# Performance work log

Measured on AMD Instinct MI355X. Metric: run time of the kernel, lower is better.

Reference implementation:

```python
import jax, jax.numpy as jnp
import numpy as np

B, N, D, DH, H, L = 32768, 6, 128, 64, 4, 4  # batch, items, dim_inp, head/ffn dim, heads, encoders
SEQ = 4  # tokens kept by embeddings[:, :4, :]
EPS = 1e-5


def _layernorm(x, g, b):
    mu = jnp.mean(x, axis=-1, keepdims=True)
    var = jnp.mean((x - mu) ** 2, axis=-1, keepdims=True)
    return (x - mu) / jnp.sqrt(var + EPS) * g + b


def setup_inputs() -> dict:
    key = jax.random.key(0)
    ks = jax.random.split(key, 18)
    s = 0.05
    f32 = jnp.float32
    return {
        "embeddings": jax.random.normal(ks[0], (B, N, D), f32),
        # per-layer, per-head QKV projections: [L, H, D, DH]
        "wq": jax.random.normal(ks[1], (L, H, D, DH), f32) * s,
        "bq": jax.random.normal(ks[2], (L, H, DH), f32) * s,
        "wk": jax.random.normal(ks[3], (L, H, D, DH), f32) * s,
        "bk": jax.random.normal(ks[4], (L, H, DH), f32) * s,
        "wv": jax.random.normal(ks[5], (L, H, D, DH), f32) * s,
        "bv": jax.random.normal(ks[6], (L, H, DH), f32) * s,
        # output projection after head concat: [L, H*DH, D]
        "wo": jax.random.normal(ks[7], (L, H * DH, D), f32) * s,
        "bo": jax.random.normal(ks[8], (L, D), f32) * s,
        "ln1_g": jnp.ones((L, D), f32),
        "ln1_b": jnp.zeros((L, D), f32),
        # FFN: Linear(D, DH) -> GELU -> Linear(DH, D)
        "ff_w1": jax.random.normal(ks[9], (L, D, DH), f32) * s,
        "ff_b1": jax.random.normal(ks[10], (L, DH), f32) * s,
        "ff_w2": jax.random.normal(ks[11], (L, DH, D), f32) * s,
        "ff_b2": jax.random.normal(ks[12], (L, D), f32) * s,
        "ln2_g": jnp.ones((L, D), f32),
        "ln2_b": jnp.zeros((L, D), f32),
    }


def reference(embeddings, wq, bq, wk, bk, wv, bv, wo, bo,
              ln1_g, ln1_b, ff_w1, ff_b1, ff_w2, ff_b2, ln2_g, ln2_b):
    x = embeddings[:, :SEQ, :]          # [B, 4, D]
    positive_pair = embeddings[:, 4, :]  # [B, D]
    negative_pairs = embeddings[:, 5:, :]  # [B, 1, D]

    # Original AttentionHead scales by sqrt(seq_len) (query.size(1)), not sqrt(head_dim)
    scale = jnp.sqrt(jnp.asarray(SEQ, x.dtype))

    for l in range(L):
        # all heads batched into one einsum (same math as per-head Linear+bmm loop)
        q = jnp.einsum('bsd,hdf->bhsf', x, wq[l]) + bq[l][:, None, :]
        k = jnp.einsum('bsd,hdf->bhsf', x, wk[l]) + bk[l][:, None, :]
        v = jnp.einsum('bsd,hdf->bhsf', x, wv[l]) + bv[l][:, None, :]
        scores = jnp.einsum('bhsf,bhtf->bhst', q, k) / scale  # [B,H,4,4]
        attn = jax.nn.softmax(scores, axis=-1)
        ctx = jnp.einsum('bhst,bhtf->bhsf', attn, v)
        # torch.cat over heads along last dim == [B,S,H,DH] -> [B,S,H*DH]
        ctx = ctx.transpose(0, 2, 1, 3).reshape(x.shape[0], SEQ, H * DH)
        proj = ctx @ wo[l] + bo[l]
        context = _layernorm(x + proj, ln1_g[l], ln1_b[l])
        # FFN (dropout = identity in eval); GELU is exact (erf) as in torch default
        h = jax.nn.gelu(context @ ff_w1[l] + ff_b1[l], approximate=False)
        res = h @ ff_w2[l] + ff_b2[l]
        # NOTE: residual uses the PRE-attention input (faithful to Encoder.forward)
        x = _layernorm(res + x, ln2_g[l], ln2_b[l])

    final_embedding = x.mean(axis=-2)  # [B, D]
    return (final_embedding, positive_pair, negative_pairs)
```

## Files before the change

kernel.cpp:

```cpp
#include <hip/hip_runtime.h>
#include <stdint.h>


typedef __attribute__((ext_vector_type(8))) short    bf16x8;
typedef __attribute__((ext_vector_type(4))) _Float16 f16x4;
typedef __attribute__((ext_vector_type(4))) float    f32x4;

#define MFMA_BF(a,b,c) __builtin_amdgcn_mfma_f32_16x16x32_bf16((a),(b),(c),0,0,0)
#define MFMA_H(a,b,c)  __builtin_amdgcn_mfma_f32_16x16x16f16((a),(b),(c),0,0,0)

__device__ __forceinline__ unsigned short f2bf(float f){
  unsigned u = __float_as_uint(f);
  u += 0x7FFFu + ((u>>16)&1u);
  return (unsigned short)(u>>16);
}
__device__ __forceinline__ unsigned pk2bf(float a, float b){
  return (unsigned)f2bf(a) | ((unsigned)f2bf(b)<<16);
}
__device__ __forceinline__ unsigned pkh(float a, float b){
  auto h = __builtin_amdgcn_cvt_pkrtz(a, b);
  return __builtin_bit_cast(unsigned, h);
}
__device__ __forceinline__ void ubf2(unsigned u, float& a, float& b){
  a = __uint_as_float(u<<16);
  b = __uint_as_float(u & 0xffff0000u);
}

__global__ __launch_bounds__(256) void prep_kernel(
    const float* __restrict__ wq, const float* __restrict__ wk,
    const float* __restrict__ wv, const float* __restrict__ wo,
    const float* __restrict__ w1, const float* __restrict__ w2,
    unsigned short* __restrict__ ws){
  int e16 = blockIdx.x*256 + threadIdx.x;
  int t    = e16 >> 10;
  int c    = (e16 >> 6) & 15;
  int lane = e16 & 63;
  int lnid = lane & 15, qid = lane >> 4;
  int l = t/18, r = t - l*18;
  float v[8];
  if (r < 16){
    int h = r >> 2, ty = r & 3;
    if (ty < 3){
      const float* W = (ty==0? wq : (ty==1? wk : wv)) + (size_t)(l*4+h)*8192;
      int f = (c>>2)*16 + lnid, d0 = (c&3)*32 + qid*8;
      #pragma unroll
      for (int j=0;j<8;++j) v[j] = W[(d0+j)*64 + f];
    } else {
      const float* W = wo + (size_t)l*32768 + (size_t)h*8192;
      int dd = (c>>1)*16 + lnid, k0 = (c&1)*32 + qid*8;
      #pragma unroll
      for (int j=0;j<8;++j) v[j] = W[(k0+j)*128 + dd];
    }
  } else if (r == 16){
    const float* W = w1 + (size_t)l*8192;
    int f = (c>>2)*16 + lnid, d0 = (c&3)*32 + qid*8;
    #pragma unroll
    for (int j=0;j<8;++j) v[j] = W[(d0+j)*64 + f];
  } else {
    const float* W = w2 + (size_t)l*8192;
    int dd = (c>>1)*16 + lnid, k0 = (c&1)*32 + qid*8;
    #pragma unroll
    for (int j=0;j<8;++j) v[j] = W[(k0+j)*128 + dd];
  }
  uint4 o;
  o.x = pk2bf(v[0],v[1]); o.y = pk2bf(v[2],v[3]);
  o.z = pk2bf(v[4],v[5]); o.w = pk2bf(v[6],v[7]);
  ((uint4*)ws)[e16] = o;
}

#define XOFF  0
#define QOFF  4352
#define KOFF  6656
#define VOFF  8960
#define PG    11520
#define WSOFF 46080
#define SLOTSZ 16384
#define LDSSZ 78848

__global__ __launch_bounds__(256,2) void bert_kernel(
    const float* __restrict__ emb,
    const float* __restrict__ bq, const float* __restrict__ bk, const float* __restrict__ bv,
    const float* __restrict__ bo,
    const float* __restrict__ ln1g, const float* __restrict__ ln1b,
    const float* __restrict__ fb1, const float* __restrict__ fb2,
    const float* __restrict__ ln2g, const float* __restrict__ ln2b,
    const unsigned short* __restrict__ ws,
    float* __restrict__ out)
{
  __shared__ __align__(16) char smem[LDSSZ];
  const int tid  = threadIdx.x;
  const int wid  = tid>>6;
  const int lane = tid&63;
  const int lnid = lane&15;
  const int qid  = lane>>4;
  const int batch0 = blockIdx.x*16;
  char* gb = smem + wid*PG;
  const f32x4 ZV = {0.f,0.f,0.f,0.f};

  {
    int row = lane>>2, colq = (lane&3)*32;
    const float* src = emb + ((size_t)(batch0 + wid*4 + (row>>2))*6 + (row&3))*128 + colq;
    #pragma unroll
    for (int i=0;i<8;++i){
      float4 v = *(const float4*)(src + i*4);
      uint2 u; u.x = pk2bf(v.x,v.y); u.y = pk2bf(v.z,v.w);
      *(uint2*)(gb + XOFF + row*272 + (colq+i*4)*2) = u;
    }
  }
  {
    const float* eb = emb + (size_t)batch0*768;
    float* o1 = out + 4194304 + (size_t)batch0*128;
    float* o2 = out + 8388608 + (size_t)batch0*128;
    #pragma unroll
    for (int i=0;i<4;++i){
      int idx = i*256 + tid;
      int b = idx>>6, rem = idx&63;
      float4 v = *(const float4*)(eb + b*768 + 512 + rem*4);
      if (rem<32) *(float4*)(o1 + b*128 + rem*4) = v;
      else        *(float4*)(o2 + b*128 + (rem-32)*4) = v;
    }
  }

  const uint4* wsv = (const uint4*)ws;
  {
    #pragma unroll
    for (int i=0;i<4;++i)
      *(uint4*)(smem + WSOFF + (i*256+tid)*16) = wsv[i*256+tid];
  }
  __syncthreads();

  f32x4  pacc[8];
  bf16x8 xfrag[4];
  f16x4  vreg[4];
  int sidx = 0;

  for (int l=0; l<4; ++l){
    #pragma unroll
    for (int kc=0;kc<4;++kc)
      xfrag[kc] = *(const bf16x8*)(gb + XOFF + lnid*272 + kc*64 + qid*16);
    #pragma unroll
    for (int nt=0;nt<8;++nt) pacc[nt] = ZV;

    for (int ph=0; ph<18; ++ph){
      char* slot = smem + WSOFF + (sidx&1)*SLOTSZ;

      uint4 pf0,pf1,pf2,pf3;
      bool havepf = (sidx+1 < 72);
      if (havepf){
        const uint4* p = wsv + (size_t)(sidx+1)*1024 + tid;
        pf0 = p[0]; pf1 = p[256]; pf2 = p[512]; pf3 = p[768];
      }

      if (ph < 16){
        int h = ph>>2, t = ph&3;
        if (t < 2){
          char* dst = gb + (t? KOFF : QOFF);
          const float* bias_base = (t? bk : bq) + (l*4+h)*64;
          #pragma unroll
          for (int nt=0; nt<4; ++nt){
            f32x4 a = ZV;
            #pragma unroll
            for (int kc=0; kc<4; ++kc){
              bf16x8 wf = *(const bf16x8*)(slot + (nt*4+kc)*1024 + lane*16);
              a = MFMA_BF(wf, xfrag[kc], a);
            }
            f32x4 bs = *(const f32x4*)(bias_base + nt*16 + qid*4);
            uint2 u; u.x = pk2bf(a[0]+bs[0], a[1]+bs[1]);
                     u.y = pk2bf(a[2]+bs[2], a[3]+bs[3]);
            *(uint2*)(dst + lnid*144 + nt*32 + qid*8) = u;
          }
        } else if (t == 2){
          const float* bias_base = bv + (l*4+h)*64;
          #pragma unroll
          for (int nt=0; nt<4; ++nt){
            f32x4 a = ZV;
            #pragma unroll
            for (int kc=0; kc<4; ++kc){
              bf16x8 wf = *(const bf16x8*)(slot + (nt*4+kc)*1024 + lane*16);
              a = MFMA_BF(xfrag[kc], wf, a);
            }
            float b = bias_base[nt*16 + lnid];
            union { unsigned u[2]; f16x4 h4; } pu;
            pu.u[0] = pkh(a[0]+b, a[1]+b);
            pu.u[1] = pkh(a[2]+b, a[3]+b);
            vreg[nt] = pu.h4;
          }
        } else {
          bf16x8 kf0 = *(const bf16x8*)(gb+KOFF + lnid*144 + qid*16);
          bf16x8 kf1 = *(const bf16x8*)(gb+KOFF + lnid*144 + 64 + qid*16);
          bf16x8 qf0 = *(const bf16x8*)(gb+QOFF + lnid*144 + qid*16);
          bf16x8 qf1 = *(const bf16x8*)(gb+QOFF + lnid*144 + 64 + qid*16);
          f32x4 st = MFMA_BF(kf0, qf0, ZV);
          st = MFMA_BF(kf1, qf1, st);
          float s0=st[0]*0.5f, s1=st[1]*0.5f, s2=st[2]*0.5f, s3=st[3]*0.5f;
          float mx = fmaxf(fmaxf(s0,s1), fmaxf(s2,s3));
          float p0=__expf(s0-mx), p1=__expf(s1-mx), p2=__expf(s2-mx), p3=__expf(s3-mx);
          float inv = 1.f/(p0+p1+p2+p3);
          bool valid = (lnid>>2) == qid;
          p0 = valid? p0*inv:0.f; p1 = valid? p1*inv:0.f;
          p2 = valid? p2*inv:0.f; p3 = valid? p3*inv:0.f;
          union { unsigned u[2]; f16x4 h4; } pu;
          pu.u[0] = pkh(p0,p1);
          pu.u[1] = pkh(p2,p3);
          f16x4 pf = pu.h4;
          #pragma unroll
          for (int ft=0; ft<4; ++ft){
            f32x4 c = MFMA_H(vreg[ft], pf, ZV);
            uint2 u; u.x = pk2bf(c[0],c[1]); u.y = pk2bf(c[2],c[3]);
            *(uint2*)(gb+QOFF + lnid*144 + ft*32 + qid*8) = u;
          }
          asm volatile("" ::: "memory");
          bf16x8 c0 = *(const bf16x8*)(gb+QOFF + lnid*144 + qid*16);
          bf16x8 c1 = *(const bf16x8*)(gb+QOFF + lnid*144 + 64 + qid*16);
          #pragma unroll
          for (int nt=0; nt<8; ++nt){
            bf16x8 w0 = *(const bf16x8*)(slot + (nt*2+0)*1024 + lane*16);
            bf16x8 w1f= *(const bf16x8*)(slot + (nt*2+1)*1024 + lane*16);
            f32x4 a = pacc[nt];
            a = MFMA_BF(w0, c0, a);
            a = MFMA_BF(w1f, c1, a);
            pacc[nt] = a;
          }
        }
      } else if (ph == 16){
        float sm=0.f, sq=0.f;
        #pragma unroll
        for (int nt=0;nt<8;++nt){
          f32x4 b4 = *(const f32x4*)(bo + l*128 + nt*16 + qid*4);
          uint2 xr = *(const uint2*)(gb+XOFF + lnid*272 + nt*32 + qid*8);
          float x0,x1,x2,x3; ubf2(xr.x,x0,x1); ubf2(xr.y,x2,x3);
          f32x4 a = pacc[nt];
          a[0]+=b4[0]+x0; a[1]+=b4[1]+x1; a[2]+=b4[2]+x2; a[3]+=b4[3]+x3;
          sm += a[0]+a[1]+a[2]+a[3];
          sq += a[0]*a[0]+a[1]*a[1]+a[2]*a[2]+a[3]*a[3];
          pacc[nt] = a;
        }
        sm += __shfl_xor(sm,16); sq += __shfl_xor(sq,16);
        sm += __shfl_xor(sm,32); sq += __shfl_xor(sq,32);
        float mu = sm*(1.f/128.f);
        float rs = rsqrtf(sq*(1.f/128.f) - mu*mu + 1e-5f);
        #pragma unroll
        for (int nt=0;nt<8;++nt){
          f32x4 g4 = *(const f32x4*)(ln1g + l*128 + nt*16 + qid*4);
          f32x4 be = *(const f32x4*)(ln1b + l*128 + nt*16 + qid*4);
          f32x4 a = pacc[nt];
          float v0 = (a[0]-mu)*rs*g4[0]+be[0];
          float v1 = (a[1]-mu)*rs*g4[1]+be[1];
          float v2 = (a[2]-mu)*rs*g4[2]+be[2];
          float v3 = (a[3]-mu)*rs*g4[3]+be[3];
          uint2 u; u.x = pk2bf(v0,v1); u.y = pk2bf(v2,v3);
          *(uint2*)(gb+QOFF + lnid*272 + nt*32 + qid*8) = u;
        }
        asm volatile("" ::: "memory");
        bf16x8 x2f[4];
        #pragma unroll
        for (int kc=0;kc<4;++kc)
          x2f[kc] = *(const bf16x8*)(gb+QOFF + lnid*272 + kc*64 + qid*16);
        #pragma unroll
        for (int nt=0; nt<4; ++nt){
          f32x4 a = ZV;
          #pragma unroll
          for (int kc=0; kc<4; ++kc){
            bf16x8 wf = *(const bf16x8*)(slot + (nt*4+kc)*1024 + lane*16);
            a = MFMA_BF(wf, x2f[kc], a);
          }
          f32x4 b1 = *(const f32x4*)(fb1 + l*64 + nt*16 + qid*4);
          float g0,g1,g2,g3;
          { float x = a[0]+b1[0]; g0 = 0.5f*x*(1.f+erff(x*0.70710678f)); }
          { float x = a[1]+b1[1]; g1 = 0.5f*x*(1.f+erff(x*0.70710678f)); }
          { float x = a[2]+b1[2]; g2 = 0.5f*x*(1.f+erff(x*0.70710678f)); }
          { float x = a[3]+b1[3]; g3 = 0.5f*x*(1.f+erff(x*0.70710678f)); }
          uint2 u; u.x = pk2bf(g0,g1); u.y = pk2bf(g2,g3);
          *(uint2*)(gb+VOFF + lnid*144 + nt*32 + qid*8) = u;
        }
      } else {
        bf16x8 h0  = *(const bf16x8*)(gb+VOFF + lnid*144 + qid*16);
        bf16x8 h1f = *(const bf16x8*)(gb+VOFF + lnid*144 + 64 + qid*16);
        f32x4 racc[8];
        #pragma unroll
        for (int nt=0; nt<8; ++nt){
          bf16x8 w0 = *(const bf16x8*)(slot + (nt*2+0)*1024 + lane*16);
          bf16x8 w1f= *(const bf16x8*)(slot + (nt*2+1)*1024 + lane*16);
          f32x4 a = MFMA_BF(w0, h0, ZV);
          a = MFMA_BF(w1f, h1f, a);
          racc[nt] = a;
        }
        float sm=0.f, sq=0.f;
        #pragma unroll
        for (int nt=0;nt<8;++nt){
          f32x4 b4 = *(const f32x4*)(fb2 + l*128 + nt*16 + qid*4);
          uint2 xr = *(const uint2*)(gb+XOFF + lnid*272 + nt*32 + qid*8);
          float x0,x1,x2,x3; ubf2(xr.x,x0,x1); ubf2(xr.y,x2,x3);
          f32x4 a = racc[nt];
          a[0]+=b4[0]+x0; a[1]+=b4[1]+x1; a[2]+=b4[2]+x2; a[3]+=b4[3]+x3;
          sm += a[0]+a[1]+a[2]+a[3];
          sq += a[0]*a[0]+a[1]*a[1]+a[2]*a[2]+a[3]*a[3];
          racc[nt] = a;
        }
        sm += __shfl_xor(sm,16); sq += __shfl_xor(sq,16);
        sm += __shfl_xor(sm,32); sq += __shfl_xor(sq,32);
        float mu = sm*(1.f/128.f);
        float rs = rsqrtf(sq*(1.f/128.f) - mu*mu + 1e-5f);
        #pragma unroll
        for (int nt=0;nt<8;++nt){
          f32x4 g4 = *(const f32x4*)(ln2g + l*128 + nt*16 + qid*4);
          f32x4 be = *(const f32x4*)(ln2b + l*128 + nt*16 + qid*4);
          f32x4 a = racc[nt];
          float v0 = (a[0]-mu)*rs*g4[0]+be[0];
          float v1 = (a[1]-mu)*rs*g4[1]+be[1];
          float v2 = (a[2]-mu)*rs*g4[2]+be[2];
          float v3 = (a[3]-mu)*rs*g4[3]+be[3];
          uint2 u; u.x = pk2bf(v0,v1); u.y = pk2bf(v2,v3);
          *(uint2*)(gb+XOFF + lnid*272 + nt*32 + qid*8) = u;
        }
      }

      if (havepf){
        char* ns = smem + WSOFF + ((sidx+1)&1)*SLOTSZ;
        uint4* q = (uint4*)(ns) + tid;
        q[0]=pf0; q[256]=pf1; q[512]=pf2; q[768]=pf3;
      }
      __syncthreads();
      ++sidx;
    }
  }

  {
    int bl = lane>>4;
    float acc[8] = {0,0,0,0,0,0,0,0};
    #pragma unroll
    for (int s=0;s<4;++s){
      uint4 u = *(const uint4*)(gb + XOFF + (bl*4+s)*272 + lnid*16);
      float a0,a1;
      ubf2(u.x,a0,a1); acc[0]+=a0; acc[1]+=a1;
      ubf2(u.y,a0,a1); acc[2]+=a0; acc[3]+=a1;
      ubf2(u.z,a0,a1); acc[4]+=a0; acc[5]+=a1;
      ubf2(u.w,a0,a1); acc[6]+=a0; acc[7]+=a1;
    }
    float* dst = out + (size_t)(batch0 + wid*4 + bl)*128 + lnid*8;
    f32x4 v0 = {acc[0]*0.25f, acc[1]*0.25f, acc[2]*0.25f, acc[3]*0.25f};
    f32x4 v1 = {acc[4]*0.25f, acc[5]*0.25f, acc[6]*0.25f, acc[7]*0.25f};
    *(f32x4*)dst = v0;
    *(f32x4*)(dst+4) = v1;
  }
}

extern "C" void kernel_launch(void* const* d_in, const int* in_sizes, int n_in,
                              void* d_out, int out_size, void* d_ws, size_t ws_size,
                              hipStream_t stream) {
  const float* emb  = (const float*)d_in[0];
  const float* wq   = (const float*)d_in[1];
  const float* bq   = (const float*)d_in[2];
  const float* wk   = (const float*)d_in[3];
  const float* bk   = (const float*)d_in[4];
  const float* wv   = (const float*)d_in[5];
  const float* bv   = (const float*)d_in[6];
  const float* wo   = (const float*)d_in[7];
  const float* bo   = (const float*)d_in[8];
  const float* ln1g = (const float*)d_in[9];
  const float* ln1b = (const float*)d_in[10];
  const float* fw1  = (const float*)d_in[11];
  const float* fb1  = (const float*)d_in[12];
  const float* fw2  = (const float*)d_in[13];
  const float* fb2  = (const float*)d_in[14];
  const float* ln2g = (const float*)d_in[15];
  const float* ln2b = (const float*)d_in[16];
  unsigned short* ws = (unsigned short*)d_ws;
  float* out = (float*)d_out;

  prep_kernel<<<288, 256, 0, stream>>>(wq, wk, wv, wo, fw1, fw2, ws);
  bert_kernel<<<2048, 256, 0, stream>>>(emb, bq, bk, bv, bo, ln1g, ln1b,
                                        fb1, fb2, ln2g, ln2b, ws, out);
}
```

Baseline: 628.3 us.

## Single-buffer weight slot and reuse Q region to fit three blocks per CU

```diff
diff --git a/kernel.cpp b/kernel.cpp
--- a/kernel.cpp
+++ b/kernel.cpp
@@ -71,13 +71,12 @@
 #define XOFF  0
 #define QOFF  4352
 #define KOFF  6656
-#define VOFF  8960
-#define PG    11520
-#define WSOFF 46080
+#define PG    8960
+#define WSOFF 35840
 #define SLOTSZ 16384
-#define LDSSZ 78848
-
-__global__ __launch_bounds__(256,2) void bert_kernel(
+#define LDSSZ 52224
+
+__global__ __launch_bounds__(256,3) void bert_kernel(
     const float* __restrict__ emb,
     const float* __restrict__ bq, const float* __restrict__ bk, const float* __restrict__ bv,
     const float* __restrict__ bo,
@@ -95,7 +94,9 @@
   const int qid  = lane>>4;
   const int batch0 = blockIdx.x*16;
   char* gb = smem + wid*PG;
+  char* slot = smem + WSOFF;
   const f32x4 ZV = {0.f,0.f,0.f,0.f};
+  const uint4* wsv = (const uint4*)ws;
 
   {
     int row = lane>>2, colq = (lane&3)*32;
@@ -120,19 +121,16 @@
       else        *(float4*)(o2 + b*128 + (rem-32)*4) = v;
     }
   }
-
-  const uint4* wsv = (const uint4*)ws;
   {
     #pragma unroll
     for (int i=0;i<4;++i)
-      *(uint4*)(smem + WSOFF + (i*256+tid)*16) = wsv[i*256+tid];
+      *(uint4*)(slot + (i*256+tid)*16) = wsv[i*256+tid];
   }
   __syncthreads();
 
   f32x4  pacc[8];
   bf16x8 xfrag[4];
   f16x4  vreg[4];
-  int sidx = 0;
 
   for (int l=0; l<4; ++l){
     #pragma unroll
@@ -142,20 +140,25 @@
     for (int nt=0;nt<8;++nt) pacc[nt] = ZV;
 
     for (int ph=0; ph<18; ++ph){
-      char* slot = smem + WSOFF + (sidx&1)*SLOTSZ;
-
-      uint4 pf0,pf1,pf2,pf3;
-      bool havepf = (sidx+1 < 72);
+      const int nxt = l*18 + ph + 1;
+      const bool havepf = (nxt < 72);
+      uint4 pf0, pf1, pf2, pf3;
       if (havepf){
-        const uint4* p = wsv + (size_t)(sidx+1)*1024 + tid;
+        const uint4* p = wsv + (size_t)nxt*1024 + tid;
         pf0 = p[0]; pf1 = p[256]; pf2 = p[512]; pf3 = p[768];
       }
+      auto commit = [&](){
+        if (havepf){
+          uint4* q = (uint4*)slot + tid;
+          q[0]=pf0; q[256]=pf1; q[512]=pf2; q[768]=pf3;
+        }
+      };
 
       if (ph < 16){
         int h = ph>>2, t = ph&3;
         if (t < 2){
-          char* dst = gb + (t? KOFF : QOFF);
           const float* bias_base = (t? bk : bq) + (l*4+h)*64;
+          f32x4 a4[4];
           #pragma unroll
           for (int nt=0; nt<4; ++nt){
             f32x4 a = ZV;
@@ -164,13 +167,22 @@
               bf16x8 wf = *(const bf16x8*)(slot + (nt*4+kc)*1024 + lane*16);
               a = MFMA_BF(wf, xfrag[kc], a);
             }
+            a4[nt] = a;
+          }
+          __syncthreads();
+          commit();
+          char* dst = gb + (t? KOFF : QOFF);
+          #pragma unroll
+          for (int nt=0; nt<4; ++nt){
             f32x4 bs = *(const f32x4*)(bias_base + nt*16 + qid*4);
-            uint2 u; u.x = pk2bf(a[0]+bs[0], a[1]+bs[1]);
-                     u.y = pk2bf(a[2]+bs[2], a[3]+bs[3]);
+            uint2 u; u.x = pk2bf(a4[nt][0]+bs[0], a4[nt][1]+bs[1]);
+                     u.y = pk2bf(a4[nt][2]+bs[2], a4[nt][3]+bs[3]);
             *(uint2*)(dst + lnid*144 + nt*32 + qid*8) = u;
           }
+          __syncthreads();
         } else if (t == 2){
           const float* bias_base = bv + (l*4+h)*64;
+          f32x4 a4[4];
           #pragma unroll
           for (int nt=0; nt<4; ++nt){
             f32x4 a = ZV;
@@ -179,12 +191,19 @@
               bf16x8 wf = *(const bf16x8*)(slot + (nt*4+kc)*1024 + lane*16);
               a = MFMA_BF(xfrag[kc], wf, a);
             }
+            a4[nt] = a;
+          }
+          __syncthreads();
+          commit();
+          #pragma unroll
+          for (int nt=0; nt<4; ++nt){
             float b = bias_base[nt*16 + lnid];
             union { unsigned u[2]; f16x4 h4; } pu;
-            pu.u[0] = pkh(a[0]+b, a[1]+b);
-            pu.u[1] = pkh(a[2]+b, a[3]+b);
+            pu.u[0] = pkh(a4[nt][0]+b, a4[nt][1]+b);
+            pu.u[1] = pkh(a4[nt][2]+b, a4[nt][3]+b);
             vreg[nt] = pu.h4;
           }
+          __syncthreads();
         } else {
           bf16x8 kf0 = *(const bf16x8*)(gb+KOFF + lnid*144 + qid*16);
           bf16x8 kf1 = *(const bf16x8*)(gb+KOFF + lnid*144 + 64 + qid*16);
@@ -221,6 +240,9 @@
             a = MFMA_BF(w1f, c1, a);
             pacc[nt] = a;
           }
+          __syncthreads();
+          commit();
+          __syncthreads();
         }
       } else if (ph == 16){
         float sm=0.f, sq=0.f;
@@ -256,6 +278,7 @@
         #pragma unroll
         for (int kc=0;kc<4;++kc)
           x2f[kc] = *(const bf16x8*)(gb+QOFF + lnid*272 + kc*64 + qid*16);
+        f32x4 f14[4];
         #pragma unroll
         for (int nt=0; nt<4; ++nt){
           f32x4 a = ZV;
@@ -264,18 +287,26 @@
             bf16x8 wf = *(const bf16x8*)(slot + (nt*4+kc)*1024 + lane*16);
             a = MFMA_BF(wf, x2f[kc], a);
           }
+          f14[nt] = a;
+        }
+        __syncthreads();
+        commit();
+        #pragma unroll
+        for (int nt=0; nt<4; ++nt){
           f32x4 b1 = *(const f32x4*)(fb1 + l*64 + nt*16 + qid*4);
+          f32x4 a = f14[nt];
           float g0,g1,g2,g3;
           { float x = a[0]+b1[0]; g0 = 0.5f*x*(1.f+erff(x*0.70710678f)); }
           { float x = a[1]+b1[1]; g1 = 0.5f*x*(1.f+erff(x*0.70710678f)); }
           { float x = a[2]+b1[2]; g2 = 0.5f*x*(1.f+erff(x*0.70710678f)); }
           { float x = a[3]+b1[3]; g3 = 0.5f*x*(1.f+erff(x*0.70710678f)); }
           uint2 u; u.x = pk2bf(g0,g1); u.y = pk2bf(g2,g3);
-          *(uint2*)(gb+VOFF + lnid*144 + nt*32 + qid*8) = u;
-        }
+          *(uint2*)(gb+QOFF + lnid*144 + nt*32 + qid*8) = u;
+        }
+        __syncthreads();
       } else {
-        bf16x8 h0  = *(const bf16x8*)(gb+VOFF + lnid*144 + qid*16);
-        bf16x8 h1f = *(const bf16x8*)(gb+VOFF + lnid*144 + 64 + qid*16);
+        bf16x8 h0  = *(const bf16x8*)(gb+QOFF + lnid*144 + qid*16);
+        bf16x8 h1f = *(const bf16x8*)(gb+QOFF + lnid*144 + 64 + qid*16);
         f32x4 racc[8];
         #pragma unroll
         for (int nt=0; nt<8; ++nt){
@@ -285,6 +316,8 @@
           a = MFMA_BF(w1f, h1f, a);
           racc[nt] = a;
         }
+        __syncthreads();
+        commit();
         float sm=0.f, sq=0.f;
         #pragma unroll
         for (int nt=0;nt<8;++nt){
@@ -313,15 +346,8 @@
           uint2 u; u.x = pk2bf(v0,v1); u.y = pk2bf(v2,v3);
           *(uint2*)(gb+XOFF + lnid*272 + nt*32 + qid*8) = u;
         }
+        __syncthreads();
       }
-
-      if (havepf){
-        char* ns = smem + WSOFF + ((sidx+1)&1)*SLOTSZ;
-        uint4* q = (uint4*)(ns) + tid;
-        q[0]=pf0; q[256]=pf1; q[512]=pf2; q[768]=pf3;
-      }
-      __syncthreads();
-      ++sidx;
     }
   }
 
```

New measurement: 1.016 ms. +61.7%, slower.
